# Kernel optimization log

Hardware: AMD Instinct MI355X
Metric: run time of the kernel (lower is better)

## Reference

```python
import jax, jax.numpy as jnp
import numpy as np

BN_EPS = 1e-5


def _sparse(x, idx, W, b):
    # x: [B, N], idx: [N, K] int, W: [N, K], b: [N]
    # out[b, j] = sum_k x[b, idx[j, k]] * W[j, k] + b[j]
    g = jnp.take(x, idx, axis=1)            # [B, N, K]
    return jnp.einsum('bjk,jk->bj', g, W) + b


def _bn_train(x, gamma, beta):
    # BatchNorm1d in training mode: batch stats, biased variance
    m = jnp.mean(x, axis=0)
    v = jnp.mean(jnp.square(x - m), axis=0)
    return gamma * (x - m) * jax.lax.rsqrt(v + BN_EPS) + beta


def setup_inputs() -> dict:
    key = jax.random.key(0)
    ks = jax.random.split(key, 12)
    B, N = 16384, 784
    s = 0.5  # modest weight scale to keep the deep reuse-chain numerically tame
    return {
        'x':    jax.random.normal(ks[0], (B, N), dtype=jnp.float32),
        'idx1': jax.random.randint(ks[1], (N, 2), 0, N, dtype=jnp.int32),
        'W1':   jax.random.normal(ks[2], (N, 2), dtype=jnp.float32) * s,
        'b1':   jax.random.normal(ks[3], (N,), dtype=jnp.float32) * 0.1,
        'idx2': jax.random.randint(ks[4], (N, 4), 0, N, dtype=jnp.int32),
        'W2':   jax.random.normal(ks[5], (N, 4), dtype=jnp.float32) * s,
        'b2':   jax.random.normal(ks[6], (N,), dtype=jnp.float32) * 0.1,
        'idx3': jax.random.randint(ks[7], (N, 8), 0, N, dtype=jnp.int32),
        'W3':   jax.random.normal(ks[8], (N, 8), dtype=jnp.float32) * s,
        'b3':   jax.random.normal(ks[9], (N,), dtype=jnp.float32) * 0.1,
        'g2':   jnp.ones((N,), dtype=jnp.float32),
        'be2':  jnp.zeros((N,), dtype=jnp.float32),
        'g3':   jnp.ones((N,), dtype=jnp.float32),
        'be3':  jnp.zeros((N,), dtype=jnp.float32),
    }


def reference(x, idx1, W1, b1, idx2, W2, b2, idx3, W3, b3, g2, be2, g3, be3):
    gelu = lambda h: jax.nn.gelu(h, approximate=False)  # torch nn.GELU default (exact)
    h = gelu(_sparse(x, idx1, W1, b1))                  # sp1 -> gelu
    h = _bn_train(gelu(_sparse(h, idx2, W2, b2)), g2, be2)   # sp2 -> gelu -> bn2
    h = _bn_train(gelu(_sparse(h, idx3, W3, b3)), g3, be3)   # sp3 -> gelu -> bn3
    h = _bn_train(gelu(_sparse(h, idx2, W2, b2)), g2, be2)   # sp2 (reused) -> gelu -> bn2
    h = jax.nn.relu(_sparse(h, idx1, W1, b1))                # sp1 (reused) -> relu
    return h
```

## Files before the change

kernel.cpp:

```cpp
#include <hip/hip_runtime.h>
#include <math.h>

static constexpr int BROWS   = 16384;
static constexpr int NC      = 784;
static constexpr int TRB     = 16;
static constexpr int THREADS = 512;
static constexpr int NBLK    = BROWS / TRB;
static constexpr int NSLOT   = 2;
static constexpr int NREP    = 4;
static constexpr float EPS   = 1e-5f;
static constexpr float INV_B = 1.0f / (float)BROWS;

#if defined(__has_builtin)
#if __has_builtin(__builtin_amdgcn_global_load_lds)
#define HAVE_ASYNC_LDS 1
#endif
#if __has_builtin(__builtin_amdgcn_rcpf)
#define HAVE_RCPF 1
#endif
#if __has_builtin(__builtin_elementwise_fma)
#define HAVE_EW_FMA 1
#endif
#endif

typedef float v2f __attribute__((ext_vector_type(2)));

__device__ __forceinline__ void stage16(const float4* g, float4* l) {
#ifdef HAVE_ASYNC_LDS
    __builtin_amdgcn_global_load_lds(
        (const __attribute__((address_space(1))) void*)g,
        (__attribute__((address_space(3))) void*)l, 16, 0, 0);
#else
    *l = *g;
#endif
}

__device__ __forceinline__ unsigned short f2b(float f) {
    union { float f; unsigned u; } v; v.f = f;
    const unsigned r = v.u + 0x7fffu + ((v.u >> 16) & 1u);
    return (unsigned short)(r >> 16);
}
__device__ __forceinline__ unsigned pack2(float lo, float hi) {
    return (unsigned)f2b(lo) | ((unsigned)f2b(hi) << 16);
}
__device__ __forceinline__ unsigned long long pack4(float a, float b, float c, float d) {
    return (unsigned long long)pack2(a, b) | ((unsigned long long)pack2(c, d) << 32);
}
__device__ __forceinline__ float fast_rcp(float x) {
#ifdef HAVE_RCPF
    return __builtin_amdgcn_rcpf(x);
#else
    return 1.0f / x;
#endif
}

__device__ __forceinline__ float gelu_f(float x) {
    const float u  = x * x;
    const float z  = x * fmaf(0.0356774081f, u, 0.7978845608f);
    const float e  = __expf(2.0f * z);
    const float r  = fast_rcp(e + 1.0f);
    const float t  = fmaf(-2.0f, r, 1.0f);
    const float hx = 0.5f * x;
    return fmaf(hx, t, hx);
}

__device__ __forceinline__ void fmaq(const unsigned long long v, const float w, v2f acc[2]) {
    const unsigned lo = (unsigned)v, hi = (unsigned)(v >> 32);
    union { unsigned u; float f; } a0, a1, b0, b1;
    a0.u = lo << 16; a1.u = lo & 0xffff0000u;
    b0.u = hi << 16; b1.u = hi & 0xffff0000u;
    const v2f a = { a0.f, a1.f }, b = { b0.f, b1.f };
    const v2f w2 = { w, w };
#ifdef HAVE_EW_FMA
    acc[0] = __builtin_elementwise_fma(a, w2, acc[0]);
    acc[1] = __builtin_elementwise_fma(b, w2, acc[1]);
#else
    acc[0] += a * w2;
    acc[1] += b * w2;
#endif
}

__global__ __launch_bounds__(THREADS, 6)
void k12(const float* __restrict__ x,
         const int* __restrict__ idx1, const float* __restrict__ W1, const float* __restrict__ b1,
         const int* __restrict__ idx2, const float* __restrict__ W2, const float* __restrict__ b2,
         unsigned long long* __restrict__ outr,
         float* __restrict__ ssum, float* __restrict__ ssq)
{
    __shared__ unsigned long long tileX[4 * NC];
    __shared__ unsigned long long tileH[4 * NC];
    const int tid  = threadIdx.x;
    const int row0 = blockIdx.x * TRB;

    #pragma unroll
    for (int slot = 0; slot < NSLOT; ++slot) {
        const int c = tid + slot * THREADS;
        if (c < NC) {
            #pragma unroll
            for (int q = 0; q < 4; ++q) {
                const size_t base = (size_t)(row0 + 4 * q) * NC + c;
                tileX[q * NC + c] = pack4(x[base], x[base + NC], x[base + 2 * NC], x[base + 3 * NC]);
            }
        }
    }
    __syncthreads();

    #pragma unroll
    for (int slot = 0; slot < NSLOT; ++slot) {
        const int j = tid + slot * THREADS;
        if (j < NC) {
            const int   c0 = idx1[2 * j], c1 = idx1[2 * j + 1];
            const float w0 = W1[2 * j],   w1 = W1[2 * j + 1], bb = b1[j];
            #pragma unroll
            for (int q = 0; q < 4; ++q) {
                v2f acc[2] = { { bb, bb }, { bb, bb } };
                fmaq(tileX[q * NC + c0], w0, acc);
                fmaq(tileX[q * NC + c1], w1, acc);
                tileH[q * NC + j] = pack4(gelu_f(acc[0].x), gelu_f(acc[0].y),
                                          gelu_f(acc[1].x), gelu_f(acc[1].y));
            }
        }
    }
    __syncthreads();

    const int rep = blockIdx.x & (NREP - 1);
    unsigned long long* dst = outr + (size_t)blockIdx.x * 4 * NC;
    #pragma unroll
    for (int slot = 0; slot < NSLOT; ++slot) {
        const int j = tid + slot * THREADS;
        if (j < NC) {
            int ji[4]; float jw[4];
            #pragma unroll
            for (int k = 0; k < 4; ++k) { ji[k] = idx2[4 * j + k]; jw[k] = W2[4 * j + k]; }
            const float jb = b2[j];
            float s1 = 0.0f, s2 = 0.0f;
            #pragma unroll
            for (int q = 0; q < 4; ++q) {
                v2f acc[2] = { { jb, jb }, { jb, jb } };
                #pragma unroll
                for (int k = 0; k < 4; ++k) fmaq(tileH[q * NC + ji[k]], jw[k], acc);
                const float u0 = gelu_f(acc[0].x), u1 = gelu_f(acc[0].y);
                const float u2 = gelu_f(acc[1].x), u3 = gelu_f(acc[1].y);
                s1 += (u0 + u1) + (u2 + u3);
                s2 = fmaf(u0, u0, fmaf(u1, u1, fmaf(u2, u2, fmaf(u3, u3, s2))));
                dst[q * NC + j] = pack4(u0, u1, u2, u3);
            }
            atomicAdd(&ssum[rep * NC + j], s1);
            atomicAdd(&ssq[rep * NC + j],  s2);
        }
    }
}

template<int K, bool FINAL>
__global__ __launch_bounds__(THREADS, 8)
void kbn(const unsigned long long* __restrict__ inr,
         const int* __restrict__ idx, const float* __restrict__ W, const float* __restrict__ bias,
         const float* __restrict__ gamma, const float* __restrict__ beta,
         const float* __restrict__ psum, const float* __restrict__ psq,
         unsigned long long* __restrict__ outr, float* __restrict__ fout,
         float* __restrict__ ssum, float* __restrict__ ssq)
{
    __shared__ unsigned long long tile[4 * NC];
    __shared__ float s_sc[NC], s_sh[NC];
    const int tid  = threadIdx.x;
    const int row0 = blockIdx.x * TRB;

    {
        const float4* src = (const float4*)(inr + (size_t)blockIdx.x * 4 * NC);
        float4*       dstl = (float4*)tile;
        for (int i = tid; i < 4 * NC / 2; i += THREADS) stage16(src + i, dstl + i);
    }
    for (int j = tid; j < NC; j += THREADS) {
        float s1 = 0.0f, s2 = 0.0f;
        #pragma unroll
        for (int r = 0; r < NREP; ++r) { s1 += psum[r * NC + j]; s2 += psq[r * NC + j]; }
        const float m   = s1 * INV_B;
        const float var = fmaf(-m, m, s2 * INV_B);
        const float sc  = gamma[j] * rsqrtf(var + EPS);
        s_sc[j] = sc;
        s_sh[j] = fmaf(-m, sc, beta[j]);
    }
    __syncthreads();

    const int rep = blockIdx.x & (NREP - 1);
    unsigned long long* dst = FINAL ? nullptr : (outr + (size_t)blockIdx.x * 4 * NC);
    #pragma unroll
    for (int slot = 0; slot < NSLOT; ++slot) {
        const int j = tid + slot * THREADS;
        if (j < NC) {
            int ji[K]; float jw[K];
            float jb = bias[j];
            #pragma unroll
            for (int k = 0; k < K; ++k) {
                const int   c = idx[K * j + k];
                const float w = W[K * j + k];
                ji[k] = c; jw[k] = w * s_sc[c]; jb = fmaf(w, s_sh[c], jb);
            }
            float s1 = 0.0f, s2 = 0.0f;
            #pragma unroll
            for (int q = 0; q < 4; ++q) {
                v2f acc[2] = { { jb, jb }, { jb, jb } };
                #pragma unroll
                for (int k = 0; k < K; ++k) fmaq(tile[q * NC + ji[k]], jw[k], acc);
                if (FINAL) {
                    fout[(size_t)(row0 + 4 * q + 0) * NC + j] = fmaxf(acc[0].x, 0.0f);
                    fout[(size_t)(row0 + 4 * q + 1) * NC + j] = fmaxf(acc[0].y, 0.0f);
                    fout[(size_t)(row0 + 4 * q + 2) * NC + j] = fmaxf(acc[1].x, 0.0f);
                    fout[(size_t)(row0 + 4 * q + 3) * NC + j] = fmaxf(acc[1].y, 0.0f);
                } else {
                    const float u0 = gelu_f(acc[0].x), u1 = gelu_f(acc[0].y);
                    const float u2 = gelu_f(acc[1].x), u3 = gelu_f(acc[1].y);
                    s1 += (u0 + u1) + (u2 + u3);
                    s2 = fmaf(u0, u0, fmaf(u1, u1, fmaf(u2, u2, fmaf(u3, u3, s2))));
                    dst[q * NC + j] = pack4(u0, u1, u2, u3);
                }
            }
            if (!FINAL) {
                atomicAdd(&ssum[rep * NC + j], s1);
                atomicAdd(&ssq[rep * NC + j],  s2);
            }
        }
    }
}

extern "C" void kernel_launch(void* const* d_in, const int* in_sizes, int n_in,
                              void* d_out, int out_size, void* d_ws, size_t ws_size,
                              hipStream_t stream)
{
    const float* x    = (const float*)d_in[0];
    const int*   idx1 = (const int*)  d_in[1];
    const float* W1   = (const float*)d_in[2];
    const float* b1   = (const float*)d_in[3];
    const int*   idx2 = (const int*)  d_in[4];
    const float* W2   = (const float*)d_in[5];
    const float* b2   = (const float*)d_in[6];
    const int*   idx3 = (const int*)  d_in[7];
    const float* W3   = (const float*)d_in[8];
    const float* b3   = (const float*)d_in[9];
    const float* g2   = (const float*)d_in[10];
    const float* be2  = (const float*)d_in[11];
    const float* g3   = (const float*)d_in[12];
    const float* be3  = (const float*)d_in[13];
    float* out = (float*)d_out;

    const size_t QN = (size_t)NBLK * 4 * NC;
    unsigned long long* r0 = (unsigned long long*)d_ws;
    unsigned long long* r1 = r0 + QN;
    float* p = (float*)(r1 + QN);
    float* sum2a = p; p += NREP * NC;  float* ssq2a = p; p += NREP * NC;
    float* sum3  = p; p += NREP * NC;  float* ssq3  = p; p += NREP * NC;
    float* sum2b = p; p += NREP * NC;  float* ssq2b = p; p += NREP * NC;

    hipMemsetAsync(sum2a, 0, 6 * NREP * NC * sizeof(float), stream);

    const dim3 grid(NBLK), blk(THREADS);

    k12<<<grid, blk, 0, stream>>>(x, idx1, W1, b1, idx2, W2, b2, r0, sum2a, ssq2a);
    kbn<8, false><<<grid, blk, 0, stream>>>(
        r0, idx3, W3, b3, g2, be2, sum2a, ssq2a, r1, nullptr, sum3, ssq3);
    kbn<4, false><<<grid, blk, 0, stream>>>(
        r1, idx2, W2, b2, g3, be3, sum3, ssq3, r0, nullptr, sum2b, ssq2b);
    kbn<2, true><<<grid, blk, 0, stream>>>(
        r0, idx1, W1, b1, g2, be2, sum2b, ssq2b, nullptr, out, nullptr, nullptr);
}
```

Baseline: 185.4 us.

## Fuse all sparse layers into one cooperative kernel with grid syncs

Replaces the four-kernel chain with a single cooperative kernel. Each block keeps its 32-row tile of packed activations in LDS across every layer, and grid-wide syncs separate the BatchNorm statistic reductions. This removes the global-memory write and read of the packed intermediates between layers, and the extra kernel launches. The BN scale and shift are folded into the next layer's weights and bias. In exchange it adds three grid barriers and relies on all 512 blocks being co-resident, falling back to the old kernels if the cooperative launch fails. The per-column statistic replicas are raised to spread atomic contention.

```diff
diff --git a/kernel.cpp b/kernel.cpp
--- a/kernel.cpp
+++ b/kernel.cpp
@@ -1,15 +1,23 @@
 #include <hip/hip_runtime.h>
+#include <hip/hip_cooperative_groups.h>
 #include <math.h>
+
+namespace cg = cooperative_groups;
 
 static constexpr int BROWS   = 16384;
 static constexpr int NC      = 784;
-static constexpr int TRB     = 16;
 static constexpr int THREADS = 512;
-static constexpr int NBLK    = BROWS / TRB;
 static constexpr int NSLOT   = 2;
-static constexpr int NREP    = 4;
+static constexpr int NREP    = 8;
 static constexpr float EPS   = 1e-5f;
 static constexpr float INV_B = 1.0f / (float)BROWS;
+
+static constexpr int TRB  = 32;
+static constexpr int NQ   = TRB / 4;
+static constexpr int NBLK = BROWS / TRB;
+
+static constexpr int TRB0  = 16;
+static constexpr int NBLK0 = BROWS / TRB0;
 
 #if defined(__has_builtin)
 #if __has_builtin(__builtin_amdgcn_global_load_lds)
@@ -80,6 +88,189 @@
 #endif
 }
 
+
+template<int K, bool FOLD, bool STATS>
+__device__ __forceinline__ void sparse_quads(
+    const unsigned long long* __restrict__ tile,
+    const float* __restrict__ s_sc, const float* __restrict__ s_sh,
+    const int* __restrict__ idx, const float* __restrict__ W,
+    const float* __restrict__ bias, const int j,
+    unsigned long long o[NQ], float& s1, float& s2)
+{
+    int ji[K]; float jw[K];
+    float jb = bias[j];
+    #pragma unroll
+    for (int k = 0; k < K; ++k) {
+        const int   c = idx[K * j + k];
+        const float w = W[K * j + k];
+        ji[k] = c;
+        if (FOLD) { jw[k] = w * s_sc[c]; jb = fmaf(w, s_sh[c], jb); }
+        else      { jw[k] = w; }
+    }
+    #pragma unroll
+    for (int q = 0; q < NQ; ++q) {
+        v2f a0[2] = { { jb, jb }, { jb, jb } };
+        v2f a1[2] = { { 0.f, 0.f }, { 0.f, 0.f } };
+        #pragma unroll
+        for (int k = 0; k < K; ++k)
+            fmaq(tile[q * NC + ji[k]], jw[k], (k & 1) ? a1 : a0);
+        const v2f r0v = a0[0] + a1[0], r1v = a0[1] + a1[1];
+        const float u0 = gelu_f(r0v.x), u1 = gelu_f(r0v.y);
+        const float u2 = gelu_f(r1v.x), u3 = gelu_f(r1v.y);
+        if (STATS) {
+            s1 += (u0 + u1) + (u2 + u3);
+            s2 = fmaf(u0, u0, fmaf(u1, u1, fmaf(u2, u2, fmaf(u3, u3, s2))));
+        }
+        o[q] = pack4(u0, u1, u2, u3);
+    }
+}
+
+__device__ __forceinline__ void writeback(unsigned long long* __restrict__ tile,
+                                          const int tid, const int j1,
+                                          const unsigned long long o0[NQ],
+                                          const unsigned long long o1[NQ])
+{
+    #pragma unroll
+    for (int q = 0; q < NQ; ++q) tile[q * NC + tid] = o0[q];
+    if (j1 < NC) {
+        #pragma unroll
+        for (int q = 0; q < NQ; ++q) tile[q * NC + j1] = o1[q];
+    }
+}
+
+__device__ __forceinline__ void finalize_bn(const float* __restrict__ psum,
+                                            const float* __restrict__ psq,
+                                            const float* __restrict__ gamma,
+                                            const float* __restrict__ beta,
+                                            float* __restrict__ s_sc,
+                                            float* __restrict__ s_sh, const int tid)
+{
+    #pragma unroll
+    for (int s = 0; s < NSLOT; ++s) {
+        const int j = tid + s * THREADS;
+        if (j < NC) {
+            float s1 = 0.f, s2 = 0.f;
+            #pragma unroll
+            for (int r = 0; r < NREP; ++r) { s1 += psum[r * NC + j]; s2 += psq[r * NC + j]; }
+            const float m   = s1 * INV_B;
+            const float var = fmaf(-m, m, s2 * INV_B);
+            const float sc  = gamma[j] * rsqrtf(var + EPS);
+            s_sc[j] = sc;
+            s_sh[j] = fmaf(-m, sc, beta[j]);
+        }
+    }
+}
+
+__global__ __launch_bounds__(THREADS, 4)
+void fused(const float* __restrict__ x,
+           const int* __restrict__ idx1, const float* __restrict__ W1, const float* __restrict__ b1,
+           const int* __restrict__ idx2, const float* __restrict__ W2, const float* __restrict__ b2,
+           const int* __restrict__ idx3, const float* __restrict__ W3, const float* __restrict__ b3,
+           const float* __restrict__ g2, const float* __restrict__ be2,
+           const float* __restrict__ g3, const float* __restrict__ be3,
+           float* __restrict__ out,
+           float* __restrict__ sum2a, float* __restrict__ ssq2a,
+           float* __restrict__ sum3,  float* __restrict__ ssq3,
+           float* __restrict__ sum2b, float* __restrict__ ssq2b)
+{
+    __shared__ unsigned long long tile[NQ * NC];
+    __shared__ float s_sc[NC], s_sh[NC];
+    cg::grid_group grid = cg::this_grid();
+
+    const int tid  = threadIdx.x;
+    const int row0 = blockIdx.x * TRB;
+    const int rep  = blockIdx.x & (NREP - 1);
+    const int j1   = tid + THREADS;
+
+    #pragma unroll
+    for (int s = 0; s < NSLOT; ++s) {
+        const int c = tid + s * THREADS;
+        if (c < NC) {
+            #pragma unroll
+            for (int q = 0; q < NQ; ++q) {
+                const size_t base = (size_t)(row0 + 4 * q) * NC + c;
+                tile[q * NC + c] = pack4(x[base], x[base + NC], x[base + 2 * NC], x[base + 3 * NC]);
+            }
+        }
+    }
+    __syncthreads();
+
+    unsigned long long o0[NQ], o1[NQ];
+    float s1a, s2a, s1b, s2b;
+
+    sparse_quads<2, false, false>(tile, s_sc, s_sh, idx1, W1, b1, tid, o0, s1a, s2a);
+    if (j1 < NC)
+        sparse_quads<2, false, false>(tile, s_sc, s_sh, idx1, W1, b1, j1, o1, s1b, s2b);
+    __syncthreads();
+    writeback(tile, tid, j1, o0, o1);
+    __syncthreads();
+
+    s1a = s2a = s1b = s2b = 0.f;
+    sparse_quads<4, false, true>(tile, s_sc, s_sh, idx2, W2, b2, tid, o0, s1a, s2a);
+    if (j1 < NC)
+        sparse_quads<4, false, true>(tile, s_sc, s_sh, idx2, W2, b2, j1, o1, s1b, s2b);
+    __syncthreads();
+    writeback(tile, tid, j1, o0, o1);
+    atomicAdd(&sum2a[rep * NC + tid], s1a); atomicAdd(&ssq2a[rep * NC + tid], s2a);
+    if (j1 < NC) { atomicAdd(&sum2a[rep * NC + j1], s1b); atomicAdd(&ssq2a[rep * NC + j1], s2b); }
+    grid.sync();
+    finalize_bn(sum2a, ssq2a, g2, be2, s_sc, s_sh, tid);
+    __syncthreads();
+
+    s1a = s2a = s1b = s2b = 0.f;
+    sparse_quads<8, true, true>(tile, s_sc, s_sh, idx3, W3, b3, tid, o0, s1a, s2a);
+    if (j1 < NC)
+        sparse_quads<8, true, true>(tile, s_sc, s_sh, idx3, W3, b3, j1, o1, s1b, s2b);
+    __syncthreads();
+    writeback(tile, tid, j1, o0, o1);
+    atomicAdd(&sum3[rep * NC + tid], s1a); atomicAdd(&ssq3[rep * NC + tid], s2a);
+    if (j1 < NC) { atomicAdd(&sum3[rep * NC + j1], s1b); atomicAdd(&ssq3[rep * NC + j1], s2b); }
+    grid.sync();
+    finalize_bn(sum3, ssq3, g3, be3, s_sc, s_sh, tid);
+    __syncthreads();
+
+    s1a = s2a = s1b = s2b = 0.f;
+    sparse_quads<4, true, true>(tile, s_sc, s_sh, idx2, W2, b2, tid, o0, s1a, s2a);
+    if (j1 < NC)
+        sparse_quads<4, true, true>(tile, s_sc, s_sh, idx2, W2, b2, j1, o1, s1b, s2b);
+    __syncthreads();
+    writeback(tile, tid, j1, o0, o1);
+    atomicAdd(&sum2b[rep * NC + tid], s1a); atomicAdd(&ssq2b[rep * NC + tid], s2a);
+    if (j1 < NC) { atomicAdd(&sum2b[rep * NC + j1], s1b); atomicAdd(&ssq2b[rep * NC + j1], s2b); }
+    grid.sync();
+    finalize_bn(sum2b, ssq2b, g2, be2, s_sc, s_sh, tid);
+    __syncthreads();
+
+    #pragma unroll
+    for (int s = 0; s < NSLOT; ++s) {
+        const int j = tid + s * THREADS;
+        if (j < NC) {
+            int ji[2]; float jw[2];
+            float jb = b1[j];
+            #pragma unroll
+            for (int k = 0; k < 2; ++k) {
+                const int   c = idx1[2 * j + k];
+                const float w = W1[2 * j + k];
+                ji[k] = c; jw[k] = w * s_sc[c]; jb = fmaf(w, s_sh[c], jb);
+            }
+            #pragma unroll
+            for (int q = 0; q < NQ; ++q) {
+                v2f a0[2] = { { jb, jb }, { jb, jb } };
+                v2f a1[2] = { { 0.f, 0.f }, { 0.f, 0.f } };
+                fmaq(tile[q * NC + ji[0]], jw[0], a0);
+                fmaq(tile[q * NC + ji[1]], jw[1], a1);
+                const v2f r0v = a0[0] + a1[0], r1v = a0[1] + a1[1];
+                const size_t base = (size_t)(row0 + 4 * q) * NC + j;
+                out[base         ] = fmaxf(r0v.x, 0.f);
+                out[base +     NC] = fmaxf(r0v.y, 0.f);
+                out[base + 2 * NC] = fmaxf(r1v.x, 0.f);
+                out[base + 3 * NC] = fmaxf(r1v.y, 0.f);
+            }
+        }
+    }
+}
+
+
 __global__ __launch_bounds__(THREADS, 6)
 void k12(const float* __restrict__ x,
          const int* __restrict__ idx1, const float* __restrict__ W1, const float* __restrict__ b1,
@@ -90,7 +281,7 @@
     __shared__ unsigned long long tileX[4 * NC];
     __shared__ unsigned long long tileH[4 * NC];
     const int tid  = threadIdx.x;
-    const int row0 = blockIdx.x * TRB;
+    const int row0 = blockIdx.x * TRB0;
 
     #pragma unroll
     for (int slot = 0; slot < NSLOT; ++slot) {
@@ -163,7 +354,7 @@
     __shared__ unsigned long long tile[4 * NC];
     __shared__ float s_sc[NC], s_sh[NC];
     const int tid  = threadIdx.x;
-    const int row0 = blockIdx.x * TRB;
+    const int row0 = blockIdx.x * TRB0;
 
     {
         const float4* src = (const float4*)(inr + (size_t)blockIdx.x * 4 * NC);
@@ -243,7 +434,7 @@
     const float* be3  = (const float*)d_in[13];
     float* out = (float*)d_out;
 
-    const size_t QN = (size_t)NBLK * 4 * NC;
+    const size_t QN = (size_t)NBLK0 * 4 * NC;
     unsigned long long* r0 = (unsigned long long*)d_ws;
     unsigned long long* r1 = r0 + QN;
     float* p = (float*)(r1 + QN);
@@ -253,8 +444,22 @@
 
     hipMemsetAsync(sum2a, 0, 6 * NREP * NC * sizeof(float), stream);
 
-    const dim3 grid(NBLK), blk(THREADS);
-
+    void* args[] = {
+        (void*)&x,
+        (void*)&idx1, (void*)&W1, (void*)&b1,
+        (void*)&idx2, (void*)&W2, (void*)&b2,
+        (void*)&idx3, (void*)&W3, (void*)&b3,
+        (void*)&g2, (void*)&be2, (void*)&g3, (void*)&be3,
+        (void*)&out,
+        (void*)&sum2a, (void*)&ssq2a,
+        (void*)&sum3,  (void*)&ssq3,
+        (void*)&sum2b, (void*)&ssq2b
+    };
+    const hipError_t err = hipLaunchCooperativeKernel(
+        (const void*)fused, dim3(NBLK), dim3(THREADS), args, 0, stream);
+    if (err == hipSuccess) return;
+
+    const dim3 grid(NBLK0), blk(THREADS);
     k12<<<grid, blk, 0, stream>>>(x, idx1, W1, b1, idx2, W2, b2, r0, sum2a, ssq2a);
     kbn<8, false><<<grid, blk, 0, stream>>>(
         r0, idx3, W3, b3, g2, be2, sum2a, ssq2a, r1, nullptr, sum3, ssq3);
```

After: 405.5 us. 119% more time.

## Replace atomic BN stat accumulation with per-block partials and a reduction kernel

Applied to the files above, without the earlier changes.

Each block now writes its per-column sum and sum-of-squares as a float2 row into a partials buffer instead of issuing atomicAdds into four replicated slots. Three new small reduction kernels (49 blocks of 16 columns each) sum the 1024 partial rows and compute the BN scale/shift once per column. The consumer kernels then only copy that precomputed scale/shift into shared memory. This removes the global atomic contention and the memset, at the cost of three extra launches, a serialized low-parallelism reduction between stages, and an extra ~6 MB of partial traffic per stage.

```diff
diff --git a/kernel.cpp b/kernel.cpp
--- a/kernel.cpp
+++ b/kernel.cpp
@@ -3,13 +3,15 @@
 
 static constexpr int BROWS   = 16384;
 static constexpr int NC      = 784;
+static constexpr int THREADS = 512;
 static constexpr int TRB     = 16;
-static constexpr int THREADS = 512;
 static constexpr int NBLK    = BROWS / TRB;
 static constexpr int NSLOT   = 2;
-static constexpr int NREP    = 4;
 static constexpr float EPS   = 1e-5f;
 static constexpr float INV_B = 1.0f / (float)BROWS;
+
+static constexpr int KRED_BLK  = 49;
+static constexpr int KRED_COLS = 16;
 
 #if defined(__has_builtin)
 #if __has_builtin(__builtin_amdgcn_global_load_lds)
@@ -85,7 +87,7 @@
          const int* __restrict__ idx1, const float* __restrict__ W1, const float* __restrict__ b1,
          const int* __restrict__ idx2, const float* __restrict__ W2, const float* __restrict__ b2,
          unsigned long long* __restrict__ outr,
-         float* __restrict__ ssum, float* __restrict__ ssq)
+         float2* __restrict__ P)
 {
     __shared__ unsigned long long tileX[4 * NC];
     __shared__ unsigned long long tileH[4 * NC];
@@ -123,8 +125,8 @@
     }
     __syncthreads();
 
-    const int rep = blockIdx.x & (NREP - 1);
     unsigned long long* dst = outr + (size_t)blockIdx.x * 4 * NC;
+    float2* prow = P + (size_t)blockIdx.x * NC;
     #pragma unroll
     for (int slot = 0; slot < NSLOT; ++slot) {
         const int j = tid + slot * THREADS;
@@ -145,9 +147,41 @@
                 s2 = fmaf(u0, u0, fmaf(u1, u1, fmaf(u2, u2, fmaf(u3, u3, s2))));
                 dst[q * NC + j] = pack4(u0, u1, u2, u3);
             }
-            atomicAdd(&ssum[rep * NC + j], s1);
-            atomicAdd(&ssq[rep * NC + j],  s2);
-        }
+            prow[j] = make_float2(s1, s2);
+        }
+    }
+}
+
+__global__ __launch_bounds__(THREADS, 8)
+void kred(const float2* __restrict__ P,
+          const float* __restrict__ gamma, const float* __restrict__ beta,
+          float2* __restrict__ scsh)
+{
+    __shared__ float redx[THREADS], redy[THREADS];
+    const int tid = threadIdx.x;
+    const int c0  = blockIdx.x * KRED_COLS;
+    const int c   = tid & (KRED_COLS - 1);
+    const int g   = tid >> 4;
+    float s1 = 0.f, s2 = 0.f;
+    const float2* base = P + (size_t)(g * 32) * NC + (c0 + c);
+    #pragma unroll 8
+    for (int r = 0; r < 32; ++r) {
+        const float2 v = base[(size_t)r * NC];
+        s1 += v.x; s2 += v.y;
+    }
+    redx[tid] = s1; redy[tid] = s2;
+    __syncthreads();
+    #pragma unroll
+    for (int off = THREADS / 2; off >= KRED_COLS; off >>= 1) {
+        if (tid < off) { redx[tid] += redx[tid + off]; redy[tid] += redy[tid + off]; }
+        __syncthreads();
+    }
+    if (tid < KRED_COLS) {
+        const int j = c0 + tid;
+        const float m   = redx[tid] * INV_B;
+        const float var = fmaf(-m, m, redy[tid] * INV_B);
+        const float sc  = gamma[j] * rsqrtf(var + EPS);
+        scsh[j] = make_float2(sc, fmaf(-m, sc, beta[j]));
     }
 }
 
@@ -155,13 +189,12 @@
 __global__ __launch_bounds__(THREADS, 8)
 void kbn(const unsigned long long* __restrict__ inr,
          const int* __restrict__ idx, const float* __restrict__ W, const float* __restrict__ bias,
-         const float* __restrict__ gamma, const float* __restrict__ beta,
-         const float* __restrict__ psum, const float* __restrict__ psq,
+         const float2* __restrict__ scsh,
          unsigned long long* __restrict__ outr, float* __restrict__ fout,
-         float* __restrict__ ssum, float* __restrict__ ssq)
+         float2* __restrict__ P)
 {
     __shared__ unsigned long long tile[4 * NC];
-    __shared__ float s_sc[NC], s_sh[NC];
+    __shared__ float2 s_f[NC];
     const int tid  = threadIdx.x;
     const int row0 = blockIdx.x * TRB;
 
@@ -170,20 +203,11 @@
         float4*       dstl = (float4*)tile;
         for (int i = tid; i < 4 * NC / 2; i += THREADS) stage16(src + i, dstl + i);
     }
-    for (int j = tid; j < NC; j += THREADS) {
-        float s1 = 0.0f, s2 = 0.0f;
-        #pragma unroll
-        for (int r = 0; r < NREP; ++r) { s1 += psum[r * NC + j]; s2 += psq[r * NC + j]; }
-        const float m   = s1 * INV_B;
-        const float var = fmaf(-m, m, s2 * INV_B);
-        const float sc  = gamma[j] * rsqrtf(var + EPS);
-        s_sc[j] = sc;
-        s_sh[j] = fmaf(-m, sc, beta[j]);
-    }
-    __syncthreads();
-
-    const int rep = blockIdx.x & (NREP - 1);
+    for (int j = tid; j < NC; j += THREADS) s_f[j] = scsh[j];
+    __syncthreads();
+
     unsigned long long* dst = FINAL ? nullptr : (outr + (size_t)blockIdx.x * 4 * NC);
+    float2* prow = FINAL ? nullptr : (P + (size_t)blockIdx.x * NC);
     #pragma unroll
     for (int slot = 0; slot < NSLOT; ++slot) {
         const int j = tid + slot * THREADS;
@@ -192,9 +216,10 @@
             float jb = bias[j];
             #pragma unroll
             for (int k = 0; k < K; ++k) {
-                const int   c = idx[K * j + k];
-                const float w = W[K * j + k];
-                ji[k] = c; jw[k] = w * s_sc[c]; jb = fmaf(w, s_sh[c], jb);
+                const int    c = idx[K * j + k];
+                const float  w = W[K * j + k];
+                const float2 f = s_f[c];
+                ji[k] = c; jw[k] = w * f.x; jb = fmaf(w, f.y, jb);
             }
             float s1 = 0.0f, s2 = 0.0f;
             #pragma unroll
@@ -215,10 +240,7 @@
                     dst[q * NC + j] = pack4(u0, u1, u2, u3);
                 }
             }
-            if (!FINAL) {
-                atomicAdd(&ssum[rep * NC + j], s1);
-                atomicAdd(&ssq[rep * NC + j],  s2);
-            }
+            if (!FINAL) prow[j] = make_float2(s1, s2);
         }
     }
 }
@@ -246,20 +268,19 @@
     const size_t QN = (size_t)NBLK * 4 * NC;
     unsigned long long* r0 = (unsigned long long*)d_ws;
     unsigned long long* r1 = r0 + QN;
-    float* p = (float*)(r1 + QN);
-    float* sum2a = p; p += NREP * NC;  float* ssq2a = p; p += NREP * NC;
-    float* sum3  = p; p += NREP * NC;  float* ssq3  = p; p += NREP * NC;
-    float* sum2b = p; p += NREP * NC;  float* ssq2b = p; p += NREP * NC;
-
-    hipMemsetAsync(sum2a, 0, 6 * NREP * NC * sizeof(float), stream);
+    float2* P     = (float2*)(r1 + QN);
+    float2* scshA = P + (size_t)NBLK * NC;
+    float2* scshB = scshA + NC;
+    float2* scshC = scshB + NC;
 
     const dim3 grid(NBLK), blk(THREADS);
-
-    k12<<<grid, blk, 0, stream>>>(x, idx1, W1, b1, idx2, W2, b2, r0, sum2a, ssq2a);
-    kbn<8, false><<<grid, blk, 0, stream>>>(
-        r0, idx3, W3, b3, g2, be2, sum2a, ssq2a, r1, nullptr, sum3, ssq3);
-    kbn<4, false><<<grid, blk, 0, stream>>>(
-        r1, idx2, W2, b2, g3, be3, sum3, ssq3, r0, nullptr, sum2b, ssq2b);
-    kbn<2, true><<<grid, blk, 0, stream>>>(
-        r0, idx1, W1, b1, g2, be2, sum2b, ssq2b, nullptr, out, nullptr, nullptr);
-}
+    const dim3 rgrid(KRED_BLK);
+
+    k12<<<grid, blk, 0, stream>>>(x, idx1, W1, b1, idx2, W2, b2, r0, P);
+    kred<<<rgrid, blk, 0, stream>>>(P, g2, be2, scshA);
+    kbn<8, false><<<grid, blk, 0, stream>>>(r0, idx3, W3, b3, scshA, r1, nullptr, P);
+    kred<<<rgrid, blk, 0, stream>>>(P, g3, be3, scshB);
+    kbn<4, false><<<grid, blk, 0, stream>>>(r1, idx2, W2, b2, scshB, r0, nullptr, P);
+    kred<<<rgrid, blk, 0, stream>>>(P, g2, be2, scshC);
+    kbn<2, true><<<grid, blk, 0, stream>>>(r0, idx1, W1, b1, scshC, nullptr, out, nullptr);
+}
```

Result: slower. 194.4 us (+4.8%).
